# Kernel tuning notes

Hardware: AMD Instinct MI355X
Metric: run time of the kernel (lower is better)

## Reference

```python
import jax, jax.numpy as jnp
import numpy as np

T, D_IN, R, D_OUT = 4096, 512, 4096, 512
LEAK = 0.9
SCALE_IN = 1.0
DENSITY = 0.5
SPECTRAL_RADIUS = 0.9


def setup_inputs() -> dict:
    key = jax.random.key(0)
    ks = jax.random.split(key, 7)
    x = jax.random.normal(ks[0], (T, D_IN), dtype=jnp.float32)
    Win_w = jax.random.uniform(ks[1], (R, D_IN), minval=-SCALE_IN, maxval=SCALE_IN, dtype=jnp.float32)
    Win_b = jax.random.uniform(ks[2], (R,), minval=-SCALE_IN, maxval=SCALE_IN, dtype=jnp.float32)
    # Wres: sparse uniform matrix rescaled to target spectral radius.
    Wres_w = jax.random.uniform(ks[3], (R, R), minval=-1.0, maxval=1.0, dtype=jnp.float32)
    mask = jax.random.bernoulli(ks[4], DENSITY, (R, R)).astype(jnp.float32)
    Wres_w = Wres_w * mask
    # spectral radius of a dense-ish random uniform matrix ~ sqrt(R*density*var), var(U[-1,1])=1/3
    approx_rho = np.sqrt(R * DENSITY / 3.0)
    Wres_w = Wres_w * (SPECTRAL_RADIUS / approx_rho)
    Nint = R + D_IN
    lim = 1.0 / np.sqrt(Nint)
    Wout_w = jax.random.uniform(ks[5], (D_OUT, Nint), minval=-lim, maxval=lim, dtype=jnp.float32)
    Wout_b = jax.random.uniform(ks[6], (D_OUT,), minval=-lim, maxval=lim, dtype=jnp.float32)
    return {"x": x, "Win_w": Win_w, "Win_b": Win_b, "Wres_w": Wres_w,
            "Wout_w": Wout_w, "Wout_b": Wout_b}


def reference(x, Win_w, Win_b, Wres_w, Wout_w, Wout_b):
    # Precompute the input projection for all timesteps (one GEMM).
    u = x @ Win_w.T + Win_b                       # (T, R)
    s0 = jnp.tanh(u[0])                           # (R,)

    def step(s, ui):
        xi = jnp.tanh(ui + Wres_w @ s)
        s_new = (1.0 - LEAK) * s + LEAK * xi      # leaky integration
        return s_new, s_new

    _, rest = jax.lax.scan(step, s0, u[1:])       # (T-1, R)
    states = jnp.concatenate([s0[None, :], rest], axis=0)  # (T, R)
    xall = jnp.concatenate([x, states], axis=1)   # (T, D_IN + R)
    yout = xall @ Wout_w.T + Wout_b               # (T, D_OUT)
    return yout
```

## Files before the change

### kernel.cpp

```cpp
#include <hip/hip_runtime.h>

#define T_STEPS 4096
#define DIN     512
#define R_DIM   4096
#define DOUT    512
#define NINT    (R_DIM + DIN)
#define NBLK    256
#define NTHR    512
#define NUNIT   2048
#define LEAKF   0.9f

typedef float f32x4 __attribute__((ext_vector_type(4)));
typedef unsigned int u32;
typedef u32 u32x2 __attribute__((ext_vector_type(2)));

__device__ __forceinline__ float fast_tanh(float x)
{
    float e = __builtin_amdgcn_exp2f(x * 2.885390081777927f);
    return 1.0f - 2.0f * __builtin_amdgcn_rcpf(1.0f + e);
}

__device__ __forceinline__ u32 f2bf(float f)
{
    u32 u = __float_as_uint(f);
    return (u + 0x7FFFu + ((u >> 16) & 1u)) >> 16;
}
__device__ __forceinline__ float bfLO(u32 u) { return __uint_as_float(u << 16); }
__device__ __forceinline__ float bfHI(u32 u) { return __uint_as_float(u & 0xFFFF0000u); }

__device__ __forceinline__ float wave_reduce2(float a0, float a1, int lane)
{
    a0 += __shfl_xor(a0, 1);
    a1 += __shfl_xor(a1, 1);
    float b = (lane & 1) ? a1 : a0;
    b += __shfl_xor(b, 2);
    b += __shfl_xor(b, 4);
    b += __shfl_xor(b, 8);
    b += __shfl_xor(b, 16);
    b += __shfl_xor(b, 32);
    return b;
}

__global__ __launch_bounds__(NTHR, 2) void esn_fused(
    const float* __restrict__ x,
    const float* __restrict__ Win_w,
    const float* __restrict__ Win_b,
    const float* __restrict__ Wres,
    const float* __restrict__ Wout_w,
    const float* __restrict__ Wout_b,
    float* __restrict__ y,
    u32x2* __restrict__ comm)
{
    const int tid  = threadIdx.x;
    const int wave = tid >> 6;
    const int lane = tid & 63;
    const int bid  = blockIdx.x;
    const int row_e = (bid << 4) + (wave << 1);

    __shared__ float s_lds[2][R_DIM];
    __shared__ float wout_lds[2 * NINT];

    {
        const float* wsrc = Wout_w + (size_t)(bid << 1) * NINT;
        for (int idx = tid; idx < 2 * NINT; idx += NTHR)
            wout_lds[idx] = wsrc[idx];
    }
    float wb = 0.f;
    if (wave < 2 && lane == 0) wb = Wout_b[(bid << 1) + wave];

    f32x4 w[2][16];
    {
        const float* wp = Wres + (size_t)row_e * R_DIM + (lane << 2);
#pragma unroll
        for (int r = 0; r < 2; ++r)
#pragma unroll
            for (int c = 0; c < 16; ++c)
                w[r][c] = *(const f32x4*)(wp + (size_t)r * R_DIM + (c << 8));
    }
    f32x4 win[2][2];
    {
        const float* ip = Win_w + (size_t)row_e * DIN + (lane << 2);
#pragma unroll
        for (int r = 0; r < 2; ++r)
#pragma unroll
            for (int c = 0; c < 2; ++c)
                win[r][c] = *(const f32x4*)(ip + (size_t)r * DIN + (c << 8));
    }
    const float bias_e = Win_b[row_e];
    const float bias_o = Win_b[row_e + 1];
    float s_old_e = 0.f, s_old_o = 0.f;

    float a0, a1;

#define PROJ(xrow)                                                        \
    {                                                                     \
        f32x4 xv0 = *(const f32x4*)((xrow) + (lane << 2));                \
        f32x4 xv1 = *(const f32x4*)((xrow) + 256 + (lane << 2));          \
        a0 = 0.f; a1 = 0.f;                                               \
        _Pragma("unroll")                                                 \
        for (int q = 0; q < 4; ++q) {                                     \
            a0 += win[0][0][q] * xv0[q] + win[0][1][q] * xv1[q];          \
            a1 += win[1][0][q] * xv0[q] + win[1][1][q] * xv1[q];          \
        }                                                                 \
    }

    {
        PROJ(x);
        float b = wave_reduce2(a0, a1, lane);
        float bx = __shfl_xor(b, 1);
        if (lane == 0) {
            float sn_e = fast_tanh(b + bias_e);
            float sn_o = fast_tanh(bx + bias_o);
            s_old_e = sn_e; s_old_o = sn_o;
            u32x2 pkt;
            pkt.x = f2bf(sn_e) | (f2bf(sn_o) << 16);
            pkt.y = 1u;
            u32x2* dst = comm + (bid << 3) + wave;
            asm volatile("global_store_dwordx2 %0, %1, off sc0 sc1"
                         :: "v"(dst), "v"(pkt) : "memory");
        }
    }
    PROJ(x + DIN);

    for (int i = 1; i <= T_STEPS; ++i) {
        const int p = (i - 1) & 1;

        {
            const u32x2* src = comm + (p * NUNIT) + (tid << 2);
            const u32 tag = (u32)i;
            u32x2 q0, q1, q2, q3;
            for (;;) {
                asm volatile("global_load_dwordx2 %0, %4, off sc0 sc1\n\t"
                             "global_load_dwordx2 %1, %5, off sc0 sc1\n\t"
                             "global_load_dwordx2 %2, %6, off sc0 sc1\n\t"
                             "global_load_dwordx2 %3, %7, off sc0 sc1\n\t"
                             "s_waitcnt vmcnt(0)"
                             : "=&v"(q0), "=&v"(q1), "=&v"(q2), "=&v"(q3)
                             : "v"(src), "v"(src + 1), "v"(src + 2), "v"(src + 3)
                             : "memory");
                u32 ok = (q0.y == tag) & (q1.y == tag) &
                         (q2.y == tag) & (q3.y == tag);
                if (ok) break;
                __builtin_amdgcn_s_sleep(1);
            }
            f32x4 lo, hi;
            lo[0] = bfLO(q0.x); lo[1] = bfHI(q0.x);
            lo[2] = bfLO(q1.x); lo[3] = bfHI(q1.x);
            hi[0] = bfLO(q2.x); hi[1] = bfHI(q2.x);
            hi[2] = bfLO(q3.x); hi[3] = bfHI(q3.x);
            *(f32x4*)&s_lds[p][tid << 3] = lo;
            *(f32x4*)&s_lds[p][(tid << 3) + 4] = hi;
        }
        __syncthreads();

        if (i < T_STEPS) {
            const f32x4* s4 = (const f32x4*)&s_lds[p][0] + lane;
            float a0b = 0.f, a1b = 0.f;
#pragma unroll
            for (int c = 0; c < 16; ++c) {
                f32x4 sv = s4[c << 6];
                a0  += w[0][c][0] * sv[0] + w[0][c][1] * sv[1];
                a0b += w[0][c][2] * sv[2] + w[0][c][3] * sv[3];
                a1  += w[1][c][0] * sv[0] + w[1][c][1] * sv[1];
                a1b += w[1][c][2] * sv[2] + w[1][c][3] * sv[3];
            }
            float b = wave_reduce2(a0 + a0b, a1 + a1b, lane);
            float bx = __shfl_xor(b, 1);
            if (lane == 0) {
                float sn_e = (1.f - LEAKF) * s_old_e + LEAKF * fast_tanh(b + bias_e);
                float sn_o = (1.f - LEAKF) * s_old_o + LEAKF * fast_tanh(bx + bias_o);
                s_old_e = sn_e; s_old_o = sn_o;
                u32x2 pkt;
                pkt.x = f2bf(sn_e) | (f2bf(sn_o) << 16);
                pkt.y = (u32)(i + 1);
                u32x2* dst = comm + ((i & 1) * NUNIT) + (bid << 3) + wave;
                asm volatile("global_store_dwordx2 %0, %1, off sc0 sc1"
                             :: "v"(dst), "v"(pkt) : "memory");
            }
        }

        if (wave < 2) {
            const float* wrow = wout_lds + wave * NINT;
            float acc = 0.f;
            {
                const float* xr = x + (size_t)(i - 1) * DIN + (lane << 3);
                f32x4 xa = *(const f32x4*)xr;
                f32x4 xb = *(const f32x4*)(xr + 4);
                const f32x4* wr4 = (const f32x4*)wrow + (lane << 1);
                f32x4 wa = wr4[0], wbv = wr4[1];
#pragma unroll
                for (int q = 0; q < 4; ++q)
                    acc += xa[q] * wa[q] + xb[q] * wbv[q];
            }
            {
                const f32x4* s4 = (const f32x4*)&s_lds[p][0] + lane;
                const f32x4* wr4 = (const f32x4*)(wrow + DIN) + lane;
#pragma unroll
                for (int c = 0; c < 16; ++c) {
                    f32x4 sv = s4[c << 6];
                    f32x4 wv = wr4[c << 6];
#pragma unroll
                    for (int q = 0; q < 4; ++q)
                        acc += sv[q] * wv[q];
                }
            }
            acc += __shfl_xor(acc, 1);
            acc += __shfl_xor(acc, 2);
            acc += __shfl_xor(acc, 4);
            acc += __shfl_xor(acc, 8);
            acc += __shfl_xor(acc, 16);
            acc += __shfl_xor(acc, 32);
            if (lane == 0)
                y[(size_t)(i - 1) * DOUT + (bid << 1) + wave] = acc + wb;
        }

        if (i + 1 < T_STEPS) PROJ(x + (size_t)(i + 1) * DIN);
    }
#undef PROJ
}

extern "C" void kernel_launch(void* const* d_in, const int* in_sizes, int n_in,
                              void* d_out, int out_size, void* d_ws, size_t ws_size,
                              hipStream_t stream) {
    const float* x      = (const float*)d_in[0];
    const float* Win_w  = (const float*)d_in[1];
    const float* Win_b  = (const float*)d_in[2];
    const float* Wres_w = (const float*)d_in[3];
    const float* Wout_w = (const float*)d_in[4];
    const float* Wout_b = (const float*)d_in[5];
    float* yp = (float*)d_out;

    u32x2* comm = (u32x2*)d_ws;

    hipMemsetAsync(d_ws, 0, 2 * NUNIT * sizeof(u32x2), stream);

    void* args[] = { (void*)&x, (void*)&Win_w, (void*)&Win_b, (void*)&Wres_w,
                     (void*)&Wout_w, (void*)&Wout_b, (void*)&yp, (void*)&comm };
    hipLaunchCooperativeKernel((void*)esn_fused, dim3(NBLK), dim3(NTHR),
                               args, 0, stream);
}
```

Before: 10.68 ms.

## Stream bf16 Wres from global each step instead of fp32 register-resident rows

Adds a pre-pass kernel that converts Wres to bf16 in the workspace. The recurrent kernel no longer keeps its two fp32 Wres rows in registers and instead reloads them as bf16 from global/L2 on every timestep. The bf16 store halves the weight footprint (32 MB total) so it may stay cache-resident, and the register pressure drops. The cost is a global load per step on the serial critical path, plus bf16 rounding of the weights. The tanh and leak update are also computed on all lanes via broadcast shuffles rather than only on lane 0.

New measurement: 22.36 ms. 2.09x slower.

```diff
diff --git a/kernel.cpp b/kernel.cpp
--- a/kernel.cpp
+++ b/kernel.cpp
@@ -13,6 +13,8 @@
 typedef float f32x4 __attribute__((ext_vector_type(4)));
 typedef unsigned int u32;
 typedef u32 u32x2 __attribute__((ext_vector_type(2)));
+typedef u32 u32x4 __attribute__((ext_vector_type(4)));
+typedef unsigned short u16;
 
 __device__ __forceinline__ float fast_tanh(float x)
 {
@@ -41,11 +43,25 @@
     return b;
 }
 
+__global__ void conv_bf16(const float* __restrict__ src, u32* __restrict__ dst,
+                          int n4)
+{
+    int idx = blockIdx.x * blockDim.x + threadIdx.x;
+    int stride = gridDim.x * blockDim.x;
+    for (int i = idx; i < n4; i += stride) {
+        f32x4 v = *(const f32x4*)(src + (size_t)i * 4);
+        u32x2 o;
+        o.x = f2bf(v[0]) | (f2bf(v[1]) << 16);
+        o.y = f2bf(v[2]) | (f2bf(v[3]) << 16);
+        *(u32x2*)(dst + (size_t)i * 2) = o;
+    }
+}
+
 __global__ __launch_bounds__(NTHR, 2) void esn_fused(
     const float* __restrict__ x,
     const float* __restrict__ Win_w,
     const float* __restrict__ Win_b,
-    const float* __restrict__ Wres,
+    const u16*   __restrict__ wres_bf,
     const float* __restrict__ Wout_w,
     const float* __restrict__ Wout_b,
     float* __restrict__ y,
@@ -68,15 +84,9 @@
     float wb = 0.f;
     if (wave < 2 && lane == 0) wb = Wout_b[(bid << 1) + wave];
 
-    f32x4 w[2][16];
-    {
-        const float* wp = Wres + (size_t)row_e * R_DIM + (lane << 2);
-#pragma unroll
-        for (int r = 0; r < 2; ++r)
-#pragma unroll
-            for (int c = 0; c < 16; ++c)
-                w[r][c] = *(const f32x4*)(wp + (size_t)r * R_DIM + (c << 8));
-    }
+    const u32* wrow0 = (const u32*)(wres_bf + (size_t)row_e * R_DIM) + (lane << 2);
+    const u32* wrow1 = (const u32*)(wres_bf + (size_t)(row_e + 1) * R_DIM) + (lane << 2);
+
     f32x4 win[2][2];
     {
         const float* ip = Win_w + (size_t)row_e * DIN + (lane << 2);
@@ -107,11 +117,12 @@
     {
         PROJ(x);
         float b = wave_reduce2(a0, a1, lane);
-        float bx = __shfl_xor(b, 1);
+        float se = __shfl(b, 0) + bias_e;
+        float so = __shfl(b, 1) + bias_o;
+        float sn_e = fast_tanh(se);
+        float sn_o = fast_tanh(so);
+        s_old_e = sn_e; s_old_o = sn_o;
         if (lane == 0) {
-            float sn_e = fast_tanh(b + bias_e);
-            float sn_o = fast_tanh(bx + bias_o);
-            s_old_e = sn_e; s_old_o = sn_o;
             u32x2 pkt;
             pkt.x = f2bf(sn_e) | (f2bf(sn_o) << 16);
             pkt.y = 1u;
@@ -154,22 +165,30 @@
         __syncthreads();
 
         if (i < T_STEPS) {
-            const f32x4* s4 = (const f32x4*)&s_lds[p][0] + lane;
+            const f32x4* sbase = (const f32x4*)&s_lds[p][0] + (lane << 1);
             float a0b = 0.f, a1b = 0.f;
 #pragma unroll
-            for (int c = 0; c < 16; ++c) {
-                f32x4 sv = s4[c << 6];
-                a0  += w[0][c][0] * sv[0] + w[0][c][1] * sv[1];
-                a0b += w[0][c][2] * sv[2] + w[0][c][3] * sv[3];
-                a1  += w[1][c][0] * sv[0] + w[1][c][1] * sv[1];
-                a1b += w[1][c][2] * sv[2] + w[1][c][3] * sv[3];
+            for (int c = 0; c < 8; ++c) {
+                u32x4 wq0 = *(const u32x4*)(wrow0 + (c << 8));
+                u32x4 wq1 = *(const u32x4*)(wrow1 + (c << 8));
+                f32x4 sa = sbase[c << 7];
+                f32x4 sb = sbase[(c << 7) + 1];
+                a0  += bfLO(wq0.x) * sa[0] + bfHI(wq0.x) * sa[1]
+                     + bfLO(wq0.y) * sa[2] + bfHI(wq0.y) * sa[3];
+                a0b += bfLO(wq0.z) * sb[0] + bfHI(wq0.z) * sb[1]
+                     + bfLO(wq0.w) * sb[2] + bfHI(wq0.w) * sb[3];
+                a1  += bfLO(wq1.x) * sa[0] + bfHI(wq1.x) * sa[1]
+                     + bfLO(wq1.y) * sa[2] + bfHI(wq1.y) * sa[3];
+                a1b += bfLO(wq1.z) * sb[0] + bfHI(wq1.z) * sb[1]
+                     + bfLO(wq1.w) * sb[2] + bfHI(wq1.w) * sb[3];
             }
             float b = wave_reduce2(a0 + a0b, a1 + a1b, lane);
-            float bx = __shfl_xor(b, 1);
+            float se = __shfl(b, 0) + bias_e;
+            float so = __shfl(b, 1) + bias_o;
+            float sn_e = (1.f - LEAKF) * s_old_e + LEAKF * fast_tanh(se);
+            float sn_o = (1.f - LEAKF) * s_old_o + LEAKF * fast_tanh(so);
+            s_old_e = sn_e; s_old_o = sn_o;
             if (lane == 0) {
-                float sn_e = (1.f - LEAKF) * s_old_e + LEAKF * fast_tanh(b + bias_e);
-                float sn_o = (1.f - LEAKF) * s_old_o + LEAKF * fast_tanh(bx + bias_o);
-                s_old_e = sn_e; s_old_o = sn_o;
                 u32x2 pkt;
                 pkt.x = f2bf(sn_e) | (f2bf(sn_o) << 16);
                 pkt.y = (u32)(i + 1);
@@ -230,11 +249,14 @@
     const float* Wout_b = (const float*)d_in[5];
     float* yp = (float*)d_out;
 
-    u32x2* comm = (u32x2*)d_ws;
+    u32x2* comm   = (u32x2*)d_ws;
+    u16*   wres_bf = (u16*)((char*)d_ws + 64 * 1024);
 
     hipMemsetAsync(d_ws, 0, 2 * NUNIT * sizeof(u32x2), stream);
-
-    void* args[] = { (void*)&x, (void*)&Win_w, (void*)&Win_b, (void*)&Wres_w,
+    conv_bf16<<<2048, 256, 0, stream>>>(Wres_w, (u32*)wres_bf,
+                                        R_DIM * R_DIM / 4);
+
+    void* args[] = { (void*)&x, (void*)&Win_w, (void*)&Win_b, (void*)&wres_bf,
                      (void*)&Wout_w, (void*)&Wout_b, (void*)&yp, (void*)&comm };
     hipLaunchCooperativeKernel((void*)esn_fused, dim3(NBLK), dim3(NTHR),
                                args, 0, stream);
```
